# Kernel optimization log

Measured on AMD Instinct MI355X. Metric: run time of the kernel, lower is better.

The kernel has to match this reference:

```python
import jax, jax.numpy as jnp
import numpy as np

C = 256
NUM_HEADS = 4
GROUPS = 32  # max(1, 256//8), divides 256
EPS = 1e-5


def setup_inputs() -> dict:
    key = jax.random.key(0)
    ks = jax.random.split(key, 7)
    B, H, W = 4, 64, 64
    s = 0.02
    return {
        "x": jax.random.normal(ks[0], (B, C, H, W), dtype=jnp.float32),
        "norm_gamma": jnp.ones((C,), jnp.float32),
        "norm_beta": jnp.zeros((C,), jnp.float32),
        "qkv_w": jax.random.normal(ks[1], (3 * C, C), jnp.float32) * s,  # 1x1 conv kernel squeezed
        "qkv_b": jax.random.normal(ks[2], (3 * C,), jnp.float32) * s,
        "proj_w": jax.random.normal(ks[3], (C, C), jnp.float32) * s,
        "proj_b": jax.random.normal(ks[4], (C,), jnp.float32) * s,
    }


def reference(x, norm_gamma, norm_beta, qkv_w, qkv_b, proj_w, proj_b):
    B, Cc, H, W = x.shape
    hd = Cc // NUM_HEADS
    scale = hd ** -0.5

    # GroupNorm over (channels-per-group, H, W)
    xg = x.reshape(B, GROUPS, Cc // GROUPS, H, W)
    mu = xg.mean(axis=(2, 3, 4), keepdims=True)
    var = xg.var(axis=(2, 3, 4), keepdims=True)
    h = ((xg - mu) * jax.lax.rsqrt(var + EPS)).reshape(B, Cc, H, W)
    h = h * norm_gamma[:, None, None] + norm_beta[:, None, None]

    # 1x1 conv QKV: [B,3C,H,W]
    qkv = jnp.einsum('bchw,oc->bohw', h, qkv_w) + qkv_b[:, None, None]
    q, k, v = jnp.split(qkv, 3, axis=1)

    def heads(t):  # [B,C,H,W] -> [B,nh,HW,hd]
        return t.reshape(B, NUM_HEADS, hd, H * W).transpose(0, 1, 3, 2)

    q, k, v = heads(q), heads(k), heads(v)
    attn = jnp.einsum('bhnd,bhmd->bhnm', q, k) * scale  # [B,nh,HW,HW]
    attn = jax.nn.softmax(attn, axis=-1)
    out = jnp.einsum('bhnm,bhmd->bhnd', attn, v)  # [B,nh,HW,hd]
    out = out.transpose(0, 1, 3, 2).reshape(B, Cc, H, W)

    out = jnp.einsum('bchw,oc->bohw', out, proj_w) + proj_b[:, None, None]
    return x + out
```

## Files before the change

kernel.cpp:

```cpp
#include <hip/hip_runtime.h>
#include <hip/hip_bf16.h>
#include <stdint.h>

typedef unsigned short u16;
typedef __attribute__((ext_vector_type(8))) short bf16x8;
typedef __attribute__((ext_vector_type(4))) float f32x4;
typedef __attribute__((ext_vector_type(16))) float f32x16;

#define HW 4096
#define CC 256
#define QSCALE 0.18033688011112042f

__device__ __forceinline__ u16 f2bf(float f) {
    union { float f; uint32_t i; } v; v.f = f;
    uint32_t x = v.i;
    return (u16)((x + 0x7fffu + ((x >> 16) & 1u)) >> 16);
}

__device__ __forceinline__ float fast_exp2(float x) {
#if __has_builtin(__builtin_amdgcn_exp2f)
    return __builtin_amdgcn_exp2f(x);
#else
    return exp2f(x);
#endif
}

__device__ __forceinline__ unsigned cvt_pk_bf16(float lo, float hi) {
    unsigned r;
    asm("v_cvt_pk_bf16_f32 %0, %1, %2" : "=v"(r) : "v"(lo), "v"(hi));
    return r;
}

__device__ __forceinline__ void plane_swap(unsigned& a, unsigned& b) {
#if __has_builtin(__builtin_amdgcn_permlane32_swap)
    auto r = __builtin_amdgcn_permlane32_swap(a, b, false, false);
    a = r[0]; b = r[1];
#else
    unsigned ax = __shfl_xor((int)a, 32);
    unsigned bx = __shfl_xor((int)b, 32);
    bool hi = (threadIdx.x & 32) != 0;
    unsigned na = hi ? bx : a;
    unsigned nb = hi ? b : ax;
    a = na; b = nb;
#endif
}

#define MFMA16(a, b, c) __builtin_amdgcn_mfma_f32_16x16x32_bf16(a, b, c, 0, 0, 0)
#define MFMA32(a, b, c) __builtin_amdgcn_mfma_f32_32x32x16_bf16(a, b, c, 0, 0, 0)

__global__ void k_wsc(const float* __restrict__ qkv_w, const float* __restrict__ proj_w,
                      const float* __restrict__ x,
                      u16* __restrict__ wqkv, u16* __restrict__ wproj, float* __restrict__ stats) {
    int bid = blockIdx.x;
    if (bid < 128) {
        int bg = bid;
        const float4* p = reinterpret_cast<const float4*>(x + (size_t)bg * 8 * HW);
        float s = 0.f, ss = 0.f;
        for (int i = 0; i < 32; ++i) {
            float4 v = p[threadIdx.x + i * 256];
            s += v.x + v.y + v.z + v.w;
            ss += v.x * v.x + v.y * v.y + v.z * v.z + v.w * v.w;
        }
        __shared__ float rs[256], rss[256];
        rs[threadIdx.x] = s; rss[threadIdx.x] = ss;
        __syncthreads();
        for (int off = 128; off > 0; off >>= 1) {
            if (threadIdx.x < off) { rs[threadIdx.x] += rs[threadIdx.x + off]; rss[threadIdx.x] += rss[threadIdx.x + off]; }
            __syncthreads();
        }
        if (threadIdx.x == 0) {
            float mu = rs[0] * (1.f / 32768.f);
            float var = rss[0] * (1.f / 32768.f) - mu * mu;
            stats[bg * 2] = mu;
            stats[bg * 2 + 1] = rsqrtf(var + 1e-5f);
        }
    } else {
        int i = (bid - 128) * 256 + threadIdx.x;
        if (i < 768 * 256) {
            int o = i >> 8;
            float sc = (o < 256) ? QSCALE : 1.0f;
            wqkv[i] = f2bf(qkv_w[i] * sc);
        }
        int j = i - 768 * 256;
        if (j >= 0 && j < 256 * 256) wproj[j] = f2bf(proj_w[j]);
    }
}

__global__ __launch_bounds__(256) void k_gnt(const float* __restrict__ x, const float* __restrict__ stats,
                                             const float* __restrict__ gamma, const float* __restrict__ beta,
                                             u16* __restrict__ h_t) {
    int bid = blockIdx.x;
    int b = bid >> 8;
    int cb = (bid >> 6) & 3;
    int nb = bid & 63;
    int t = threadIdx.x;
    int cl = t >> 2;
    int ch = t & 3;
    int c = cb * 64 + cl;
    int g = c >> 3;
    float mu = stats[(b * 32 + g) * 2];
    float rsg = stats[(b * 32 + g) * 2 + 1];
    float ga = gamma[c], be = beta[c];
    __shared__ float T[64][66];
    const float4* p = reinterpret_cast<const float4*>(x + ((size_t)(b * CC + c)) * HW + nb * 64 + ch * 16);
    for (int j = 0; j < 4; ++j) {
        float4 v = p[j];
        int nbase = ch * 16 + j * 4;
        T[nbase + 0][cl] = (v.x - mu) * rsg * ga + be;
        T[nbase + 1][cl] = (v.y - mu) * rsg * ga + be;
        T[nbase + 2][cl] = (v.z - mu) * rsg * ga + be;
        T[nbase + 3][cl] = (v.w - mu) * rsg * ga + be;
    }
    __syncthreads();
    int nl = t >> 2;
    union { u16 u[16]; uint4 q[2]; } pk;
    for (int j = 0; j < 16; ++j) pk.u[j] = f2bf(T[nl][ch * 16 + j]);
    u16* dst = h_t + ((size_t)b * HW + nb * 64 + nl) * CC + cb * 64 + ch * 16;
    *reinterpret_cast<uint4*>(dst) = pk.q[0];
    *reinterpret_cast<uint4*>(dst + 8) = pk.q[1];
}

__global__ __launch_bounds__(256) void k_qkv(const u16* __restrict__ wqkv, const u16* __restrict__ h_t,
                                             const float* __restrict__ qkv_b,
                                             u16* __restrict__ qk_t, u16* __restrict__ v_o) {
    int bid = blockIdx.x;
    int b = bid / 192;
    int rem = bid % 192;
    int om = rem >> 5;
    int nb = rem & 31;
    int o0 = om * 128, n0 = nb * 128;
    int t = threadIdx.x;
    int wid = t >> 6, lane = t & 63;
    int wm = wid >> 1, wn = wid & 1;
    int l15 = lane & 15, lg = lane >> 4;

    __shared__ u16 sA[128 * 40], sB[128 * 40];
    f32x4 acc[4][4];
    for (int i = 0; i < 4; ++i) for (int j = 0; j < 4; ++j) acc[i][j] = (f32x4)0.f;

    const u16* gA = wqkv + (size_t)o0 * 256;
    const u16* gB = h_t + ((size_t)b * HW + n0) * CC;
    int row = t >> 1, half = t & 1;

    for (int kt = 0; kt < 8; ++kt) {
        __syncthreads();
        {
            const uint4* pa = reinterpret_cast<const uint4*>(gA + (size_t)row * 256 + kt * 32 + half * 16);
            uint4 a0 = pa[0], a1 = pa[1];
            const uint4* pb = reinterpret_cast<const uint4*>(gB + (size_t)row * 256 + kt * 32 + half * 16);
            uint4 b0 = pb[0], b1 = pb[1];
            *reinterpret_cast<uint4*>(&sA[row * 40 + half * 16]) = a0;
            *reinterpret_cast<uint4*>(&sA[row * 40 + half * 16 + 8]) = a1;
            *reinterpret_cast<uint4*>(&sB[row * 40 + half * 16]) = b0;
            *reinterpret_cast<uint4*>(&sB[row * 40 + half * 16 + 8]) = b1;
        }
        __syncthreads();
        bf16x8 af[4], bfr[4];
        for (int mt = 0; mt < 4; ++mt)
            af[mt] = *reinterpret_cast<const bf16x8*>(&sA[(wm * 64 + mt * 16 + l15) * 40 + lg * 8]);
        for (int nt = 0; nt < 4; ++nt)
            bfr[nt] = *reinterpret_cast<const bf16x8*>(&sB[(wn * 64 + nt * 16 + l15) * 40 + lg * 8]);
        for (int mt = 0; mt < 4; ++mt)
            for (int nt = 0; nt < 4; ++nt)
                acc[mt][nt] = MFMA16(af[mt], bfr[nt], acc[mt][nt]);
    }

    if (o0 < 512) {
        for (int mt = 0; mt < 4; ++mt) {
            int ob = o0 + wm * 64 + mt * 16 + lg * 4;
            float bias[4];
            for (int r = 0; r < 4; ++r) {
                int o = ob + r;
                bias[r] = qkv_b[o] * (o < 256 ? QSCALE : 1.0f);
            }
            for (int nt = 0; nt < 4; ++nt) {
                int n = n0 + wn * 64 + nt * 16 + l15;
                union { u16 u[4]; uint2 q; } pk;
                for (int r = 0; r < 4; ++r) pk.u[r] = f2bf(acc[mt][nt][r] + bias[r]);
                *reinterpret_cast<uint2*>(qk_t + ((size_t)b * HW + n) * 512 + ob) = pk.q;
            }
        }
    } else {
        for (int mt = 0; mt < 4; ++mt) {
            int ob = o0 + wm * 64 + mt * 16 + lg * 4;
            for (int nt = 0; nt < 4; ++nt) {
                int n = n0 + wn * 64 + nt * 16 + l15;
                for (int r = 0; r < 4; ++r) {
                    int o = ob + r;
                    float bias = qkv_b[o];
                    v_o[((size_t)b * 256 + (o - 512)) * HW + n] = f2bf(acc[mt][nt][r] + bias);
                }
            }
        }
    }
}

__global__ __launch_bounds__(512, 4) void k_attn(const u16* __restrict__ qk_t, const u16* __restrict__ v_o,
                                                 u16* __restrict__ ao_t) {
    int bid = blockIdx.x;
    int swz = (bid & 7) * 64 + (bid >> 3);
    int qb = swz & 31, head = (swz >> 5) & 3, b = swz >> 7;
    int n0 = qb * 128;
    int t = threadIdx.x;
    int kg = t >> 8;
    int wq = (t >> 6) & 3;
    int lane = t & 63, l31 = lane & 31, h = lane >> 5;

    __shared__ u16 lds[2 * 2 * 2 * 64 * 72];

    const u16* qbase = qk_t + ((size_t)b * HW + n0 + wq * 32 + l31) * 512 + head * 64 + h * 8;
    bf16x8 qf[4];
#pragma unroll
    for (int cs = 0; cs < 4; ++cs) qf[cs] = *reinterpret_cast<const bf16x8*>(qbase + cs * 16);

    const u16* gK = qk_t + (size_t)b * HW * 512 + 256 + head * 64;
    const u16* gV = v_o + ((size_t)b * 256 + head * 64) * (size_t)HW;

    int tIn = t & 255;
    int srow = tIn >> 3, sch = tIn & 7;
    const u16* pk0 = gK + (size_t)(kg * 2048 + srow) * 512 + sch * 8;
    const u16* pk1 = pk0 + 32 * 512;
    const u16* pv0 = gV + (size_t)srow * HW + kg * 2048 + sch * 8;
    const u16* pv1 = pv0 + 32 * HW;
    uint4 rk0 = *reinterpret_cast<const uint4*>(pk0);
    uint4 rk1 = *reinterpret_cast<const uint4*>(pk1);
    uint4 rv0 = *reinterpret_cast<const uint4*>(pv0);
    uint4 rv1 = *reinterpret_cast<const uint4*>(pv1);

    f32x16 o0 = (f32x16)0.f, o1 = (f32x16)0.f;
    float l_run = 0.f;
    u16* gb = lds + kg * 18432;

    for (int ti = 0; ti < 32; ++ti) {
        u16* bK = gb + (ti & 1) * 9216;
        u16* bV = bK + 4608;
        *reinterpret_cast<uint4*>(bK + srow * 72 + sch * 8) = rk0;
        *reinterpret_cast<uint4*>(bK + (srow + 32) * 72 + sch * 8) = rk1;
        *reinterpret_cast<uint4*>(bV + srow * 72 + sch * 8) = rv0;
        *reinterpret_cast<uint4*>(bV + (srow + 32) * 72 + sch * 8) = rv1;
        __syncthreads();

        if (ti < 31) {
            pk0 += 64 * 512; pk1 += 64 * 512; pv0 += 64; pv1 += 64;
            rk0 = *reinterpret_cast<const uint4*>(pk0);
            rk1 = *reinterpret_cast<const uint4*>(pk1);
            rv0 = *reinterpret_cast<const uint4*>(pv0);
            rv1 = *reinterpret_cast<const uint4*>(pv1);
        }

        f32x16 s0 = (f32x16)0.f, s1 = (f32x16)0.f;
        __builtin_amdgcn_s_setprio(1);
#pragma unroll
        for (int cs = 0; cs < 4; ++cs) {
            bf16x8 k0 = *reinterpret_cast<const bf16x8*>(bK + l31 * 72 + cs * 16 + h * 8);
            bf16x8 k1 = *reinterpret_cast<const bf16x8*>(bK + (l31 + 32) * 72 + cs * 16 + h * 8);
            s0 = MFMA32(k0, qf[cs], s0);
            s1 = MFMA32(k1, qf[cs], s1);
        }
        __builtin_amdgcn_s_setprio(0);

        float ps = 0.f;
#pragma unroll
        for (int i = 0; i < 16; ++i) { float e = fast_exp2(s0[i]); s0[i] = e; ps += e; }
#pragma unroll
        for (int i = 0; i < 16; ++i) { float e = fast_exp2(s1[i]); s1[i] = e; ps += e; }
        l_run += ps;

        unsigned dws[2][8];
#pragma unroll
        for (int a = 0; a < 4; ++a) {
            dws[0][2 * a]     = cvt_pk_bf16(s0[4 * a],     s0[4 * a + 1]);
            dws[0][2 * a + 1] = cvt_pk_bf16(s0[4 * a + 2], s0[4 * a + 3]);
            dws[1][2 * a]     = cvt_pk_bf16(s1[4 * a],     s1[4 * a + 1]);
            dws[1][2 * a + 1] = cvt_pk_bf16(s1[4 * a + 2], s1[4 * a + 3]);
        }
        bf16x8 pf[4];
#pragma unroll
        for (int ks = 0; ks < 4; ++ks) {
            int kt = ks >> 1, sf = ks & 1;
            unsigned A0 = dws[kt][4 * sf + 0], B0 = dws[kt][4 * sf + 2];
            unsigned A1 = dws[kt][4 * sf + 1], B1 = dws[kt][4 * sf + 3];
            plane_swap(A0, B0);
            plane_swap(A1, B1);
            union { unsigned d[4]; bf16x8 v; } u;
            u.d[0] = A0; u.d[1] = A1; u.d[2] = B0; u.d[3] = B1;
            pf[ks] = u.v;
        }

        __builtin_amdgcn_s_setprio(1);
#pragma unroll
        for (int ks = 0; ks < 4; ++ks) {
            bf16x8 v0 = *reinterpret_cast<const bf16x8*>(bV + l31 * 72 + ks * 16 + h * 8);
            bf16x8 v1 = *reinterpret_cast<const bf16x8*>(bV + (l31 + 32) * 72 + ks * 16 + h * 8);
            o0 = MFMA32(v0, pf[ks], o0);
            o1 = MFMA32(v1, pf[ks], o1);
        }
        __builtin_amdgcn_s_setprio(0);
    }

    l_run += __shfl_xor(l_run, 32);

    float* Of = (float*)lds;
    float* Lf = (float*)lds + 8192;
    u16* E = lds + 18432;

    __syncthreads();
    if (kg == 1) {
#pragma unroll
        for (int i = 0; i < 16; ++i) {
            Of[wq * 2048 + i * 64 + lane] = o0[i];
            Of[wq * 2048 + (16 + i) * 64 + lane] = o1[i];
        }
        Lf[wq * 64 + lane] = l_run;
    }
    __syncthreads();
    if (kg == 0) {
#pragma unroll
        for (int i = 0; i < 16; ++i) {
            o0[i] += Of[wq * 2048 + i * 64 + lane];
            o1[i] += Of[wq * 2048 + (16 + i) * 64 + lane];
        }
        l_run += Lf[wq * 64 + lane];
        float inv = 1.0f / l_run;
        int qrow = wq * 32 + l31;
#pragma unroll
        for (int r = 0; r < 16; ++r) {
            int d = (r & 3) + 8 * (r >> 2) + 4 * h;
            E[qrow * 72 + d]      = f2bf(o0[r] * inv);
            E[qrow * 72 + 32 + d] = f2bf(o1[r] * inv);
        }
    }
    __syncthreads();
#pragma unroll
    for (int i = 0; i < 2; ++i) {
        int item = i * 512 + t;
        int row = item >> 3, cb = item & 7;
        uint4 w = *reinterpret_cast<const uint4*>(E + row * 72 + cb * 8);
        *reinterpret_cast<uint4*>(ao_t + ((size_t)b * HW + n0 + row) * 256 + head * 64 + cb * 8) = w;
    }
}

__global__ __launch_bounds__(256) void k_proj(const u16* __restrict__ wproj, const u16* __restrict__ ao_t,
                                              const float* __restrict__ proj_b, const float* __restrict__ x,
                                              float* __restrict__ out) {
    int bid = blockIdx.x;
    int b = bid >> 6;
    int om = (bid >> 5) & 1;
    int nb = bid & 31;
    int o0 = om * 128, n0 = nb * 128;
    int t = threadIdx.x;
    int wid = t >> 6, lane = t & 63;
    int wm = wid >> 1, wn = wid & 1;
    int l15 = lane & 15, lg = lane >> 4;

    __shared__ u16 sA[128 * 40], sB[128 * 40];
    f32x4 acc[4][4];
    for (int i = 0; i < 4; ++i) for (int j = 0; j < 4; ++j) acc[i][j] = (f32x4)0.f;

    const u16* gA = wproj + (size_t)o0 * 256;
    const u16* gB = ao_t + ((size_t)b * HW + n0) * CC;
    int row = t >> 1, half = t & 1;

    for (int kt = 0; kt < 8; ++kt) {
        __syncthreads();
        {
            const uint4* pa = reinterpret_cast<const uint4*>(gA + (size_t)row * 256 + kt * 32 + half * 16);
            uint4 a0 = pa[0], a1 = pa[1];
            const uint4* pb = reinterpret_cast<const uint4*>(gB + (size_t)row * 256 + kt * 32 + half * 16);
            uint4 b0 = pb[0], b1 = pb[1];
            *reinterpret_cast<uint4*>(&sA[row * 40 + half * 16]) = a0;
            *reinterpret_cast<uint4*>(&sA[row * 40 + half * 16 + 8]) = a1;
            *reinterpret_cast<uint4*>(&sB[row * 40 + half * 16]) = b0;
            *reinterpret_cast<uint4*>(&sB[row * 40 + half * 16 + 8]) = b1;
        }
        __syncthreads();
        bf16x8 af[4], bfr[4];
        for (int mt = 0; mt < 4; ++mt)
            af[mt] = *reinterpret_cast<const bf16x8*>(&sA[(wm * 64 + mt * 16 + l15) * 40 + lg * 8]);
        for (int nt = 0; nt < 4; ++nt)
            bfr[nt] = *reinterpret_cast<const bf16x8*>(&sB[(wn * 64 + nt * 16 + l15) * 40 + lg * 8]);
        for (int mt = 0; mt < 4; ++mt)
            for (int nt = 0; nt < 4; ++nt)
                acc[mt][nt] = MFMA16(af[mt], bfr[nt], acc[mt][nt]);
    }

    for (int mt = 0; mt < 4; ++mt) {
        int ob = o0 + wm * 64 + mt * 16 + lg * 4;
        for (int nt = 0; nt < 4; ++nt) {
            int n = n0 + wn * 64 + nt * 16 + l15;
            for (int r = 0; r < 4; ++r) {
                int o = ob + r;
                size_t idx = ((size_t)(b * CC + o)) * HW + n;
                out[idx] = acc[mt][nt][r] + proj_b[o] + x[idx];
            }
        }
    }
}

extern "C" void kernel_launch(void* const* d_in, const int* in_sizes, int n_in,
                              void* d_out, int out_size, void* d_ws, size_t ws_size,
                              hipStream_t stream) {
    const float* x      = (const float*)d_in[0];
    const float* gamma  = (const float*)d_in[1];
    const float* beta   = (const float*)d_in[2];
    const float* qkv_w  = (const float*)d_in[3];
    const float* qkv_b  = (const float*)d_in[4];
    const float* proj_w = (const float*)d_in[5];
    const float* proj_b = (const float*)d_in[6];
    float* out = (float*)d_out;
    char* ws = (char*)d_ws;

    float* stats = (float*)ws;
    u16* wqkv  = (u16*)(ws + 4096);
    u16* wproj = (u16*)(ws + 4096 + 393216);
    u16* h_t   = (u16*)(ws + 1048576);
    u16* qk_t  = (u16*)(ws + 1048576 + 8388608);
    u16* v_o   = (u16*)(ws + 1048576 + 8388608 + 16777216);
    u16* ao_t  = (u16*)(ws + 1048576 + 8388608 + 16777216 + 8388608);

    k_wsc<<<dim3(1152), dim3(256), 0, stream>>>(qkv_w, proj_w, x, wqkv, wproj, stats);
    k_gnt<<<dim3(1024), dim3(256), 0, stream>>>(x, stats, gamma, beta, h_t);
    k_qkv<<<dim3(768), dim3(256), 0, stream>>>(wqkv, h_t, qkv_b, qk_t, v_o);
    k_attn<<<dim3(512), dim3(512), 0, stream>>>(qk_t, v_o, ao_t);
    k_proj<<<dim3(256), dim3(256), 0, stream>>>(wproj, ao_t, proj_b, x, out);
}
```

Baseline: 128.9 us.

## Pre-swizzle V into MFMA fragment layout and split GroupNorm stats reduction

The QKV kernel now writes V in a layout already tiled to match the MFMA operand fragments. The attention kernel can then load V operands directly from global memory into registers, skipping the LDS staging, which halves LDS use and cuts LDS traffic. Separately, the GroupNorm statistics pass is split across 8x more blocks that write partial sums, which the normalize kernel then combines, to raise parallelism in that pre-pass. The trade-offs are scattered 2-byte V stores in the QKV epilogue, global-latency-bound V loads inside the attention loop, and an extra barrier in the epilogue.

```diff
diff --git a/kernel.cpp b/kernel.cpp
--- a/kernel.cpp
+++ b/kernel.cpp
@@ -52,11 +52,11 @@
                       const float* __restrict__ x,
                       u16* __restrict__ wqkv, u16* __restrict__ wproj, float* __restrict__ stats) {
     int bid = blockIdx.x;
-    if (bid < 128) {
-        int bg = bid;
-        const float4* p = reinterpret_cast<const float4*>(x + (size_t)bg * 8 * HW);
+    if (bid < 1024) {
+        int bg = bid >> 3, slab = bid & 7;
+        const float4* p = reinterpret_cast<const float4*>(x + (size_t)bg * 32768 + slab * 4096);
         float s = 0.f, ss = 0.f;
-        for (int i = 0; i < 32; ++i) {
+        for (int i = 0; i < 4; ++i) {
             float4 v = p[threadIdx.x + i * 256];
             s += v.x + v.y + v.z + v.w;
             ss += v.x * v.x + v.y * v.y + v.z * v.z + v.w * v.w;
@@ -69,13 +69,11 @@
             __syncthreads();
         }
         if (threadIdx.x == 0) {
-            float mu = rs[0] * (1.f / 32768.f);
-            float var = rss[0] * (1.f / 32768.f) - mu * mu;
-            stats[bg * 2] = mu;
-            stats[bg * 2 + 1] = rsqrtf(var + 1e-5f);
+            stats[bid * 2] = rs[0];
+            stats[bid * 2 + 1] = rss[0];
         }
     } else {
-        int i = (bid - 128) * 256 + threadIdx.x;
+        int i = (bid - 1024) * 256 + threadIdx.x;
         if (i < 768 * 256) {
             int o = i >> 8;
             float sc = (o < 256) ? QSCALE : 1.0f;
@@ -98,8 +96,14 @@
     int ch = t & 3;
     int c = cb * 64 + cl;
     int g = c >> 3;
-    float mu = stats[(b * 32 + g) * 2];
-    float rsg = stats[(b * 32 + g) * 2 + 1];
+    float sum = 0.f, ssum = 0.f;
+    for (int s = 0; s < 8; ++s) {
+        sum  += stats[((b * 32 + g) * 8 + s) * 2];
+        ssum += stats[((b * 32 + g) * 8 + s) * 2 + 1];
+    }
+    float mu = sum * (1.f / 32768.f);
+    float var = ssum * (1.f / 32768.f) - mu * mu;
+    float rsg = rsqrtf(var + 1e-5f);
     float ga = gamma[c], be = beta[c];
     __shared__ float T[64][66];
     const float4* p = reinterpret_cast<const float4*>(x + ((size_t)(b * CC + c)) * HW + nb * 64 + ch * 16);
@@ -122,7 +126,7 @@
 
 __global__ __launch_bounds__(256) void k_qkv(const u16* __restrict__ wqkv, const u16* __restrict__ h_t,
                                              const float* __restrict__ qkv_b,
-                                             u16* __restrict__ qk_t, u16* __restrict__ v_o) {
+                                             u16* __restrict__ qk_t, u16* __restrict__ v_t) {
     int bid = blockIdx.x;
     int b = bid / 192;
     int rem = bid % 192;
@@ -185,17 +189,21 @@
             int ob = o0 + wm * 64 + mt * 16 + lg * 4;
             for (int nt = 0; nt < 4; ++nt) {
                 int n = n0 + wn * 64 + nt * 16 + l15;
+                int kt = n >> 6, nn = n & 63;
+                int ks = nn >> 4, hh = (nn >> 3) & 1, sub = nn & 7;
                 for (int r = 0; r < 4; ++r) {
                     int o = ob + r;
+                    int head = (o - 512) >> 6, d = (o - 512) & 63;
                     float bias = qkv_b[o];
-                    v_o[((size_t)b * 256 + (o - 512)) * HW + n] = f2bf(acc[mt][nt][r] + bias);
+                    size_t idx = (((((size_t)b * 4 + head) * 64 + kt) * 4 + ks) * 64 + d) * 16 + hh * 8 + sub;
+                    v_t[idx] = f2bf(acc[mt][nt][r] + bias);
                 }
             }
         }
     }
 }
 
-__global__ __launch_bounds__(512, 4) void k_attn(const u16* __restrict__ qk_t, const u16* __restrict__ v_o,
+__global__ __launch_bounds__(512, 4) void k_attn(const u16* __restrict__ qk_t, const u16* __restrict__ v_t,
                                                  u16* __restrict__ ao_t) {
     int bid = blockIdx.x;
     int swz = (bid & 7) * 64 + (bid >> 3);
@@ -206,7 +214,7 @@
     int wq = (t >> 6) & 3;
     int lane = t & 63, l31 = lane & 31, h = lane >> 5;
 
-    __shared__ u16 lds[2 * 2 * 2 * 64 * 72];
+    __shared__ u16 lds[2 * 2 * 64 * 72];
 
     const u16* qbase = qk_t + ((size_t)b * HW + n0 + wq * 32 + l31) * 512 + head * 64 + h * 8;
     bf16x8 qf[4];
@@ -214,38 +222,35 @@
     for (int cs = 0; cs < 4; ++cs) qf[cs] = *reinterpret_cast<const bf16x8*>(qbase + cs * 16);
 
     const u16* gK = qk_t + (size_t)b * HW * 512 + 256 + head * 64;
-    const u16* gV = v_o + ((size_t)b * 256 + head * 64) * (size_t)HW;
+    const u16* gV = v_t + ((size_t)(b * 4 + head)) * 262144 + l31 * 16 + h * 8;
 
     int tIn = t & 255;
-    int srow = tIn >> 3, sch = tIn & 7;
-    const u16* pk0 = gK + (size_t)(kg * 2048 + srow) * 512 + sch * 8;
-    const u16* pk1 = pk0 + 32 * 512;
-    const u16* pv0 = gV + (size_t)srow * HW + kg * 2048 + sch * 8;
-    const u16* pv1 = pv0 + 32 * HW;
-    uint4 rk0 = *reinterpret_cast<const uint4*>(pk0);
-    uint4 rk1 = *reinterpret_cast<const uint4*>(pk1);
-    uint4 rv0 = *reinterpret_cast<const uint4*>(pv0);
-    uint4 rv1 = *reinterpret_cast<const uint4*>(pv1);
+    int srow = tIn >> 2, q4 = tIn & 3;
+    const u16* pK = gK + (size_t)(kg * 2048 + srow) * 512 + q4 * 16;
+    uint4 rk0 = *reinterpret_cast<const uint4*>(pK);
+    uint4 rk1 = *reinterpret_cast<const uint4*>(pK + 8);
 
     f32x16 o0 = (f32x16)0.f, o1 = (f32x16)0.f;
     float l_run = 0.f;
-    u16* gb = lds + kg * 18432;
+    u16* gb = lds + kg * 9216;
 
     for (int ti = 0; ti < 32; ++ti) {
-        u16* bK = gb + (ti & 1) * 9216;
-        u16* bV = bK + 4608;
-        *reinterpret_cast<uint4*>(bK + srow * 72 + sch * 8) = rk0;
-        *reinterpret_cast<uint4*>(bK + (srow + 32) * 72 + sch * 8) = rk1;
-        *reinterpret_cast<uint4*>(bV + srow * 72 + sch * 8) = rv0;
-        *reinterpret_cast<uint4*>(bV + (srow + 32) * 72 + sch * 8) = rv1;
-        __syncthreads();
+        u16* bK = gb + (ti & 1) * 4608;
+        u16* wr = bK + srow * 72 + q4 * 16;
+        *reinterpret_cast<uint4*>(wr) = rk0;
+        *reinterpret_cast<uint4*>(wr + 8) = rk1;
+        __syncthreads();
+
+        int ktv = (kg * 32 + ti) * 4;
+        bf16x8 vf0[4];
+#pragma unroll
+        for (int ks = 0; ks < 4; ++ks)
+            vf0[ks] = *reinterpret_cast<const bf16x8*>(gV + (size_t)(ktv + ks) * 1024);
 
         if (ti < 31) {
-            pk0 += 64 * 512; pk1 += 64 * 512; pv0 += 64; pv1 += 64;
-            rk0 = *reinterpret_cast<const uint4*>(pk0);
-            rk1 = *reinterpret_cast<const uint4*>(pk1);
-            rv0 = *reinterpret_cast<const uint4*>(pv0);
-            rv1 = *reinterpret_cast<const uint4*>(pv1);
+            pK += 64 * 512;
+            rk0 = *reinterpret_cast<const uint4*>(pK);
+            rk1 = *reinterpret_cast<const uint4*>(pK + 8);
         }
 
         f32x16 s0 = (f32x16)0.f, s1 = (f32x16)0.f;
@@ -287,14 +292,16 @@
             pf[ks] = u.v;
         }
 
+        bf16x8 vf1[4];
+#pragma unroll
+        for (int ks = 0; ks < 4; ++ks)
+            vf1[ks] = *reinterpret_cast<const bf16x8*>(gV + (size_t)(ktv + ks) * 1024 + 512);
+
         __builtin_amdgcn_s_setprio(1);
 #pragma unroll
-        for (int ks = 0; ks < 4; ++ks) {
-            bf16x8 v0 = *reinterpret_cast<const bf16x8*>(bV + l31 * 72 + ks * 16 + h * 8);
-            bf16x8 v1 = *reinterpret_cast<const bf16x8*>(bV + (l31 + 32) * 72 + ks * 16 + h * 8);
-            o0 = MFMA32(v0, pf[ks], o0);
-            o1 = MFMA32(v1, pf[ks], o1);
-        }
+        for (int ks = 0; ks < 4; ++ks) o0 = MFMA32(vf0[ks], pf[ks], o0);
+#pragma unroll
+        for (int ks = 0; ks < 4; ++ks) o1 = MFMA32(vf1[ks], pf[ks], o1);
         __builtin_amdgcn_s_setprio(0);
     }
 
@@ -302,7 +309,7 @@
 
     float* Of = (float*)lds;
     float* Lf = (float*)lds + 8192;
-    u16* E = lds + 18432;
+    u16* E = lds;
 
     __syncthreads();
     if (kg == 1) {
@@ -314,6 +321,7 @@
         Lf[wq * 64 + lane] = l_run;
     }
     __syncthreads();
+    float inv = 0.f;
     if (kg == 0) {
 #pragma unroll
         for (int i = 0; i < 16; ++i) {
@@ -321,7 +329,10 @@
             o1[i] += Of[wq * 2048 + (16 + i) * 64 + lane];
         }
         l_run += Lf[wq * 64 + lane];
-        float inv = 1.0f / l_run;
+        inv = 1.0f / l_run;
+    }
+    __syncthreads();
+    if (kg == 0) {
         int qrow = wq * 32 + l31;
 #pragma unroll
         for (int r = 0; r < 16; ++r) {
@@ -411,16 +422,16 @@
     char* ws = (char*)d_ws;
 
     float* stats = (float*)ws;
-    u16* wqkv  = (u16*)(ws + 4096);
-    u16* wproj = (u16*)(ws + 4096 + 393216);
+    u16* wqkv  = (u16*)(ws + 8192);
+    u16* wproj = (u16*)(ws + 8192 + 393216);
     u16* h_t   = (u16*)(ws + 1048576);
     u16* qk_t  = (u16*)(ws + 1048576 + 8388608);
-    u16* v_o   = (u16*)(ws + 1048576 + 8388608 + 16777216);
+    u16* v_t   = (u16*)(ws + 1048576 + 8388608 + 16777216);
     u16* ao_t  = (u16*)(ws + 1048576 + 8388608 + 16777216 + 8388608);
 
-    k_wsc<<<dim3(1152), dim3(256), 0, stream>>>(qkv_w, proj_w, x, wqkv, wproj, stats);
+    k_wsc<<<dim3(2048), dim3(256), 0, stream>>>(qkv_w, proj_w, x, wqkv, wproj, stats);
     k_gnt<<<dim3(1024), dim3(256), 0, stream>>>(x, stats, gamma, beta, h_t);
-    k_qkv<<<dim3(768), dim3(256), 0, stream>>>(wqkv, h_t, qkv_b, qk_t, v_o);
-    k_attn<<<dim3(512), dim3(512), 0, stream>>>(qk_t, v_o, ao_t);
+    k_qkv<<<dim3(768), dim3(256), 0, stream>>>(wqkv, h_t, qkv_b, qk_t, v_t);
+    k_attn<<<dim3(512), dim3(512), 0, stream>>>(qk_t, v_t, ao_t);
     k_proj<<<dim3(256), dim3(256), 0, stream>>>(wproj, ao_t, proj_b, x, out);
 }
```

Measured after the change: 147.6 us. +14.5%, slower.
